# Optimization experiments

Measured on AMD Instinct MI355X. Metric: run time of the kernel, lower is better.

Reference implementation:

```python
import jax, jax.numpy as jnp
import numpy as np

N = 50000
E = 800000
IN_C = 128
HID = 16
HEADS = 8
OUT_C = 128
NEG_SLOPE = 0.2
EPS = 1e-16


def setup_inputs() -> dict:
    key = jax.random.key(0)
    ks = jax.random.split(key, 12)
    x = jax.random.normal(ks[0], (N, IN_C), dtype=jnp.float32)
    edge_index = jax.random.randint(ks[1], (2, E), 0, N, dtype=jnp.int32)
    s1 = 1.0 / np.sqrt(IN_C)
    s2 = 1.0 / np.sqrt(HID * HEADS)
    W1 = jax.random.normal(ks[2], (IN_C, HEADS * HID), dtype=jnp.float32) * s1
    att_src1 = jax.random.normal(ks[3], (HEADS, HID), dtype=jnp.float32) * s1
    att_dst1 = jax.random.normal(ks[4], (HEADS, HID), dtype=jnp.float32) * s1
    b1 = jnp.zeros((HEADS * HID,), dtype=jnp.float32)
    W2 = jax.random.normal(ks[5], (HEADS * HID, OUT_C), dtype=jnp.float32) * s2
    att_src2 = jax.random.normal(ks[6], (1, OUT_C), dtype=jnp.float32) * s2
    att_dst2 = jax.random.normal(ks[7], (1, OUT_C), dtype=jnp.float32) * s2
    b2 = jnp.zeros((OUT_C,), dtype=jnp.float32)
    return {"x": x, "edge_index": edge_index, "W1": W1, "att_src1": att_src1,
            "att_dst1": att_dst1, "b1": b1, "W2": W2, "att_src2": att_src2,
            "att_dst2": att_dst2, "b2": b2}


def _add_self_loops(edge_index, n):
    loop = jnp.arange(n, dtype=edge_index.dtype)
    src = jnp.concatenate([edge_index[0], loop])
    dst = jnp.concatenate([edge_index[1], loop])
    return src, dst


def gat_conv(x, src, dst, W, att_src, att_dst, bias, heads, out_c, concat):
    n = x.shape[0]
    h = (x @ W).reshape(n, heads, out_c)          # [N, H, C]
    a_src = jnp.einsum('nhc,hc->nh', h, att_src)  # [N, H]
    a_dst = jnp.einsum('nhc,hc->nh', h, att_dst)
    e = a_src[src] + a_dst[dst]                   # [E', H]
    e = jax.nn.leaky_relu(e, NEG_SLOPE)
    # segment softmax over edges grouped by destination node
    m = jax.ops.segment_max(e, dst, num_segments=n)          # [N, H]
    m = jnp.where(jnp.isfinite(m), m, 0.0)
    ex = jnp.exp(e - m[dst])                                  # [E', H]
    denom = jax.ops.segment_sum(ex, dst, num_segments=n)      # [N, H]
    alpha = ex / (denom[dst] + EPS)                            # [E', H]
    msg = alpha[:, :, None] * h[src]                           # [E', H, C]
    out = jax.ops.segment_sum(msg, dst, num_segments=n)       # [N, H, C]
    if concat:
        out = out.reshape(n, heads * out_c)
    else:
        out = out.mean(axis=1)
    return out + bias


def reference(x, edge_index, W1, att_src1, att_dst1, b1, W2, att_src2, att_dst2, b2):
    src, dst = _add_self_loops(edge_index, N)
    h = gat_conv(x, src, dst, W1, att_src1, att_dst1, b1, HEADS, HID, True)
    h = jax.nn.relu(h)
    # dropout is identity in eval mode
    out = gat_conv(h, src, dst, W2, att_src2, att_dst2, b2, 1, OUT_C, False)
    return out
```

## Files before the change

### kernel.cpp

```cpp
#include <hip/hip_runtime.h>


constexpr int N_NODES = 50000;
constexpr int E_EDGES = 800000;
constexpr int ETOT = E_EDGES + N_NODES;
constexpr float NEG_SLOPE = 0.2f;
constexpr float EPS = 1e-16f;
constexpr int SCAN_BLK = 512;
constexpr int NBLK_SCAN = (N_NODES + SCAN_BLK - 1) / SCAN_BLK;

typedef short bf16x8 __attribute__((ext_vector_type(8)));
typedef float f32x4 __attribute__((ext_vector_type(4)));

__device__ __forceinline__ float lrelu(float x) { return x > 0.f ? x : NEG_SLOPE * x; }
__device__ __forceinline__ ushort f2bf(float f) {
    uint u = __float_as_uint(f);
    return (ushort)((u + 0x7fffu + ((u >> 16) & 1u)) >> 16);
}
__device__ __forceinline__ float bf2f(uint u) { return __uint_as_float(u << 16); }

__device__ __forceinline__ void fma8(float* acc, uint4 p, float w, float& ws) {
    ws += w;
    acc[0] += w * bf2f(p.x & 0xffffu); acc[1] += w * bf2f(p.x >> 16);
    acc[2] += w * bf2f(p.y & 0xffffu); acc[3] += w * bf2f(p.y >> 16);
    acc[4] += w * bf2f(p.z & 0xffffu); acc[5] += w * bf2f(p.z >> 16);
    acc[6] += w * bf2f(p.w & 0xffffu); acc[7] += w * bf2f(p.w >> 16);
}

__global__ __launch_bounds__(256) void convert_W(const float* __restrict__ W1,
                                                 const float* __restrict__ W2,
                                                 const float* __restrict__ attS2,
                                                 const float* __restrict__ attD2,
                                                 ushort* __restrict__ W1t,
                                                 ushort* __restrict__ W2t,
                                                 float* __restrict__ vs,
                                                 float* __restrict__ vd,
                                                 uint* __restrict__ cnt16) {
    const int t = threadIdx.x;
    if (blockIdx.x >= 2) {
        const int i = (blockIdx.x - 2) * 256 + t;
        if (i < (N_NODES + 1) / 2) cnt16[i] = 0;
        return;
    }
    const float* W = (blockIdx.x == 0) ? W1 : W2;
    ushort* Wt = (blockIdx.x == 0) ? W1t : W2t;
    const int n = t >> 1, k0 = (t & 1) * 64;
    for (int k = 0; k < 64; k += 2) {
        uint lo = f2bf(W[(size_t)(k0 + k) * 128 + n]);
        uint hi = f2bf(W[(size_t)(k0 + k + 1) * 128 + n]);
        *(uint*)&Wt[(size_t)n * 128 + k0 + k] = lo | (hi << 16);
    }
    if (blockIdx.x == 1) {
        const int k = t & 127;
        const float* av = (t < 128) ? attS2 : attD2;
        float* dst = (t < 128) ? vs : vd;
        float s = 0.f;
        for (int c = 0; c < 128; ++c) s += W2[(size_t)k * 128 + c] * av[c];
        dst[k] = s;
    }
}

__device__ __forceinline__ uint cnt_at(const uint* cnt16, int i) {
    return (cnt16[i >> 1] >> ((i & 1) * 16)) & 0xffffu;
}

__global__ __launch_bounds__(SCAN_BLK) void block_sums(const uint* __restrict__ cnt16,
                                                       int* __restrict__ bsum) {
    __shared__ int sm[SCAN_BLK];
    int i = blockIdx.x * SCAN_BLK + threadIdx.x;
    sm[threadIdx.x] = (i < N_NODES) ? (int)cnt_at(cnt16, i) : 0;
    __syncthreads();
    for (int off = SCAN_BLK / 2; off > 0; off >>= 1) {
        if (threadIdx.x < off) sm[threadIdx.x] += sm[threadIdx.x + off];
        __syncthreads();
    }
    if (threadIdx.x == 0) bsum[blockIdx.x] = sm[0];
}

__global__ __launch_bounds__(SCAN_BLK) void scan_final_fused(const uint* __restrict__ cnt16,
                                                             const int* __restrict__ bsum,
                                                             int* __restrict__ rowptr) {
    __shared__ int sb[128];
    __shared__ int sm[SCAN_BLK];
    const int t = threadIdx.x;
    if (t < 128) sb[t] = (t < NBLK_SCAN) ? bsum[t] : 0;
    __syncthreads();
    for (int off = 1; off < 128; off <<= 1) {
        int v = 0;
        if (t < 128 && t >= off) v = sb[t - off];
        __syncthreads();
        if (t < 128) sb[t] += v;
        __syncthreads();
    }
    const int bid = blockIdx.x;
    const int bpre = sb[bid] - bsum[bid];

    const int i = bid * SCAN_BLK + t;
    const int v = (i < N_NODES) ? (int)cnt_at(cnt16, i) : 0;
    sm[t] = v;
    __syncthreads();
    for (int off = 1; off < SCAN_BLK; off <<= 1) {
        int x = (t >= off) ? sm[t - off] : 0;
        __syncthreads();
        sm[t] += x;
        __syncthreads();
    }
    if (i < N_NODES) rowptr[i] = bpre + sm[t] - v;
    if (bid == 0 && t == 0) rowptr[N_NODES] = ETOT;
}

__global__ __launch_bounds__(256) void scatter_kernel(const int* __restrict__ ei,
                                                      const int* __restrict__ rowptr,
                                                      const ushort* __restrict__ rank,
                                                      int* __restrict__ csrc) {
    int e = blockIdx.x * blockDim.x + threadIdx.x;
    if (e >= ETOT) return;
    int s, d;
    if (e < E_EDGES) { s = ei[e]; d = ei[E_EDGES + e]; }
    else             { s = d = e - E_EDGES; }
    const int pos = rowptr[d] + (int)rank[e];
    __builtin_nontemporal_store(s, &csrc[pos]);
}

template <bool BF16IN, bool ATT8, bool ATTIN>
__global__ __launch_bounds__(256) void mfma_gemm(const void* __restrict__ Xv,
                                                 const ushort* __restrict__ Wt,
                                                 ushort* __restrict__ H,
                                                 const float* __restrict__ attS,
                                                 const float* __restrict__ attD,
                                                 float* __restrict__ aS,
                                                 float* __restrict__ aD,
                                                 const int* __restrict__ ei,
                                                 uint* __restrict__ cnt16,
                                                 ushort* __restrict__ rank,
                                                 int cblocks, int nrows) {
    __shared__ __align__(16) char smem[16384 + 32768];
    ushort* lx = (ushort*)smem;
    ushort* lw = (ushort*)(smem + 16384);
    float*  hs = (float*)smem;

    const int t = threadIdx.x;

    if (blockIdx.x < cblocks) {
        const int e = blockIdx.x * 256 + t;
        if (e < ETOT) {
            const int d = (e < E_EDGES) ? ei[E_EDGES + e] : (e - E_EDGES);
            const uint shift = (d & 1) * 16;
            const uint old = atomicAdd(&cnt16[d >> 1], 1u << shift);
            rank[e] = (ushort)((old >> shift) & 0xffffu);
        }
        return;
    }

    const int r0 = (blockIdx.x - cblocks) * 64;

    {
        const int n = t >> 1, half = t & 1;
        const ushort* src = Wt + (size_t)n * 128 + half * 64;
        #pragma unroll
        for (int c = 0; c < 8; ++c) {
            int cx = half * 8 + c;
            uint4 v = *(const uint4*)(src + c * 8);
            *(uint4*)&lw[(n * 16 + (cx ^ (n & 7))) * 8] = v;
        }
    }
    {
        const int r = t >> 2, q = t & 3;
        const int grow = r0 + r;
        const uint4 z = {0, 0, 0, 0};
        #pragma unroll
        for (int cc = 0; cc < 4; ++cc) {
            int cx = q * 4 + cc;
            uint4 packed = z;
            if (grow < nrows) {
                if (BF16IN) {
                    packed = *(const uint4*)((const ushort*)Xv + (size_t)grow * 128 + cx * 8);
                } else {
                    const float* X = (const float*)Xv;
                    const float4 f0 = *(const float4*)(X + (size_t)grow * 128 + cx * 8);
                    const float4 f1 = *(const float4*)(X + (size_t)grow * 128 + cx * 8 + 4);
                    packed.x = (uint)f2bf(f0.x) | ((uint)f2bf(f0.y) << 16);
                    packed.y = (uint)f2bf(f0.z) | ((uint)f2bf(f0.w) << 16);
                    packed.z = (uint)f2bf(f1.x) | ((uint)f2bf(f1.y) << 16);
                    packed.w = (uint)f2bf(f1.z) | ((uint)f2bf(f1.w) << 16);
                }
            }
            *(uint4*)&lx[(r * 16 + (cx ^ (r & 7))) * 8] = packed;
        }
    }
    __syncthreads();

    const int wv = t >> 6, l = t & 63;
    const int row = wv * 16 + (l & 15);
    const int lg = l >> 4;
    f32x4 acc[8] = {};

    #pragma unroll
    for (int kb = 0; kb < 4; ++kb) {
        const int cx = kb * 4 + lg;
        bf16x8 a = *(const bf16x8*)&lx[(row * 16 + (cx ^ (row & 7))) * 8];
        #pragma unroll
        for (int nt = 0; nt < 8; ++nt) {
            const int n = nt * 16 + (l & 15);
            bf16x8 b = *(const bf16x8*)&lw[(n * 16 + (cx ^ (n & 7))) * 8];
            acc[nt] = __builtin_amdgcn_mfma_f32_16x16x32_bf16(a, b, acc[nt], 0, 0, 0);
        }
    }

    #pragma unroll
    for (int reg = 0; reg < 4; ++reg) {
        const int grow = r0 + wv * 16 + lg * 4 + reg;
        if (grow < nrows) {
            #pragma unroll
            for (int nt = 0; nt < 8; ++nt)
                H[(size_t)grow * 128 + nt * 16 + (l & 15)] = f2bf(acc[nt][reg]);
        }
    }

    if (ATT8) {
        __syncthreads();
        #pragma unroll
        for (int reg = 0; reg < 4; ++reg) {
            const int r = wv * 16 + lg * 4 + reg;
            #pragma unroll
            for (int nt = 0; nt < 8; ++nt)
                hs[r * 130 + nt * 16 + (l & 15)] = acc[nt][reg];
        }
        __syncthreads();
        for (int q = t; q < 512; q += 256) {
            const int r = q >> 3, h = q & 7;
            if (r0 + r < nrows) {
                float sv = 0.f, dv = 0.f;
                #pragma unroll
                for (int j = 0; j < 16; ++j) {
                    const float hv = hs[r * 130 + h * 16 + j];
                    sv += hv * attS[h * 16 + j];
                    dv += hv * attD[h * 16 + j];
                }
                aS[(size_t)(r0 + r) * 8 + h] = sv;
                aD[(size_t)(r0 + r) * 8 + h] = dv;
            }
        }
    }

    if (ATTIN) {
        const int r = t >> 2, qq = t & 3;
        float ps = 0.f, pd = 0.f;
        #pragma unroll
        for (int cc = 0; cc < 4; ++cc) {
            const int cx = qq * 4 + cc;
            const uint4 p = *(const uint4*)&lx[(r * 16 + (cx ^ (r & 7))) * 8];
            const uint w[4] = {p.x, p.y, p.z, p.w};
            #pragma unroll
            for (int q = 0; q < 4; ++q) {
                const float e0 = bf2f(w[q] & 0xffffu);
                const float e1 = bf2f(w[q] >> 16);
                ps += e0 * attS[cx * 8 + 2 * q] + e1 * attS[cx * 8 + 2 * q + 1];
                pd += e0 * attD[cx * 8 + 2 * q] + e1 * attD[cx * 8 + 2 * q + 1];
            }
        }
        ps += __shfl_xor(ps, 1); ps += __shfl_xor(ps, 2);
        pd += __shfl_xor(pd, 1); pd += __shfl_xor(pd, 2);
        if (qq == 0 && r0 + r < nrows) { aS[r0 + r] = ps; aD[r0 + r] = pd; }
    }
}

#define GISSUE(P, JJ)                                                          \
    {                                                                          \
        const int jx_ = (JJ);                                                  \
        const int sx_ = __shfl(s_l, jx_ & 63);                                 \
        P = zero4;                                                             \
        if (jx_ < rem) P = *(const uint4*)(Hm + (size_t)sx_ * 128 + i * 8);    \
    }

__global__ __launch_bounds__(256) void agg8(const int* __restrict__ rowptr,
                                            const int* __restrict__ csrc,
                                            const float* __restrict__ aS,
                                            const float* __restrict__ aD,
                                            const ushort* __restrict__ Hm,
                                            const float* __restrict__ bias,
                                            ushort* __restrict__ o1bf) {
    __shared__ float wlds[4][512];
    const int wv = threadIdx.x >> 6;
    const int d = blockIdx.x * 4 + wv;
    const int lane = threadIdx.x & 63;
    const int g = lane >> 4, i = lane & 15, hc = i >> 1;
    const int hw = lane & 7;
    const float adh = aD[(size_t)d * 8 + hw];

    const int base = rowptr[d], end = rowptr[d + 1];
    float acc[8] = {0.f, 0.f, 0.f, 0.f, 0.f, 0.f, 0.f, 0.f};
    float ws = 0.f;
    const uint4 zero4 = {0, 0, 0, 0};

    for (int c0 = base; c0 < end; c0 += 64) {
        const int rem = min(64, end - c0);
        const int s_l = (lane < rem) ? csrc[c0 + lane] : 0;

        uint4 p0, p1, p2, p3;
        GISSUE(p0, g); GISSUE(p1, g + 4); GISSUE(p2, g + 8); GISSUE(p3, g + 12);

        const int nwc = (rem + 7) >> 3;
        for (int jj = 0; jj < nwc; ++jj) {
            const int j = jj * 8 + (lane >> 3);
            const int sj = __shfl(s_l, j & 63);
            float w = 0.f;
            if (j < rem) w = __expf(lrelu(aS[(size_t)sj * 8 + hw] + adh));
            wlds[wv][j * 8 + hw] = w;
        }

        const int niter = (rem + 3) >> 2;
        for (int tb = 0; tb < niter; tb += 4) {
            const int j0 = 4 * tb + g;
            {
                const float w = (j0 < rem) ? wlds[wv][j0 * 8 + hc] : 0.f;
                fma8(acc, p0, w, ws);
                GISSUE(p0, j0 + 16);
            }
            {
                const int j1 = j0 + 4;
                const float w = (j1 < rem) ? wlds[wv][j1 * 8 + hc] : 0.f;
                fma8(acc, p1, w, ws);
                GISSUE(p1, j1 + 16);
            }
            {
                const int j2 = j0 + 8;
                const float w = (j2 < rem) ? wlds[wv][j2 * 8 + hc] : 0.f;
                fma8(acc, p2, w, ws);
                GISSUE(p2, j2 + 16);
            }
            {
                const int j3 = j0 + 12;
                const float w = (j3 < rem) ? wlds[wv][j3 * 8 + hc] : 0.f;
                fma8(acc, p3, w, ws);
                GISSUE(p3, j3 + 16);
            }
        }
    }

    #pragma unroll
    for (int k = 0; k < 8; ++k) {
        acc[k] += __shfl_xor(acc[k], 16);
        acc[k] += __shfl_xor(acc[k], 32);
    }
    ws += __shfl_xor(ws, 16);
    ws += __shfl_xor(ws, 32);

    if (g == 0) {
        const float inv = 1.f / (ws + EPS);
        float v[8];
        #pragma unroll
        for (int k = 0; k < 8; ++k) v[k] = fmaxf(acc[k] * inv + bias[i * 8 + k], 0.f);
        uint4 pk;
        pk.x = (uint)f2bf(v[0]) | ((uint)f2bf(v[1]) << 16);
        pk.y = (uint)f2bf(v[2]) | ((uint)f2bf(v[3]) << 16);
        pk.z = (uint)f2bf(v[4]) | ((uint)f2bf(v[5]) << 16);
        pk.w = (uint)f2bf(v[6]) | ((uint)f2bf(v[7]) << 16);
        *(uint4*)(o1bf + (size_t)d * 128 + i * 8) = pk;
    }
}

__global__ __launch_bounds__(256) void agg1(const int* __restrict__ rowptr,
                                            const int* __restrict__ csrc,
                                            const float* __restrict__ aS,
                                            const float* __restrict__ aD,
                                            const ushort* __restrict__ Hm,
                                            const float* __restrict__ bias,
                                            float* __restrict__ out) {
    const int wv = threadIdx.x >> 6;
    const int d = blockIdx.x * 4 + wv;
    const int lane = threadIdx.x & 63;
    const int g = lane >> 4, i = lane & 15;
    const float ad = aD[d];

    const int base = rowptr[d], end = rowptr[d + 1];
    float acc[8] = {0.f, 0.f, 0.f, 0.f, 0.f, 0.f, 0.f, 0.f};
    float ws = 0.f;
    const uint4 zero4 = {0, 0, 0, 0};

    for (int c0 = base; c0 < end; c0 += 64) {
        const int rem = min(64, end - c0);
        const int s_l = (lane < rem) ? csrc[c0 + lane] : 0;

        uint4 p0, p1, p2, p3;
        GISSUE(p0, g); GISSUE(p1, g + 4); GISSUE(p2, g + 8); GISSUE(p3, g + 12);

        const float w_l = (lane < rem) ? __expf(lrelu(aS[s_l] + ad)) : 0.f;

        const int niter = (rem + 3) >> 2;
        for (int tb = 0; tb < niter; tb += 4) {
            const int j0 = 4 * tb + g;
            {
                const float wr = __shfl(w_l, j0 & 63);
                const float w = (j0 < rem) ? wr : 0.f;
                fma8(acc, p0, w, ws);
                GISSUE(p0, j0 + 16);
            }
            {
                const int j1 = j0 + 4;
                const float wr = __shfl(w_l, j1 & 63);
                const float w = (j1 < rem) ? wr : 0.f;
                fma8(acc, p1, w, ws);
                GISSUE(p1, j1 + 16);
            }
            {
                const int j2 = j0 + 8;
                const float wr = __shfl(w_l, j2 & 63);
                const float w = (j2 < rem) ? wr : 0.f;
                fma8(acc, p2, w, ws);
                GISSUE(p2, j2 + 16);
            }
            {
                const int j3 = j0 + 12;
                const float wr = __shfl(w_l, j3 & 63);
                const float w = (j3 < rem) ? wr : 0.f;
                fma8(acc, p3, w, ws);
                GISSUE(p3, j3 + 16);
            }
        }
    }

    #pragma unroll
    for (int k = 0; k < 8; ++k) {
        acc[k] += __shfl_xor(acc[k], 16);
        acc[k] += __shfl_xor(acc[k], 32);
    }
    ws += __shfl_xor(ws, 16);
    ws += __shfl_xor(ws, 32);

    if (g == 0) {
        const float inv = 1.f / (ws + EPS);
        float4 o0, o1v;
        o0.x = acc[0] * inv + bias[i * 8 + 0];
        o0.y = acc[1] * inv + bias[i * 8 + 1];
        o0.z = acc[2] * inv + bias[i * 8 + 2];
        o0.w = acc[3] * inv + bias[i * 8 + 3];
        o1v.x = acc[4] * inv + bias[i * 8 + 4];
        o1v.y = acc[5] * inv + bias[i * 8 + 5];
        o1v.z = acc[6] * inv + bias[i * 8 + 6];
        o1v.w = acc[7] * inv + bias[i * 8 + 7];
        *(float4*)(out + (size_t)d * 128 + i * 8) = o0;
        *(float4*)(out + (size_t)d * 128 + i * 8 + 4) = o1v;
    }
}

extern "C" void kernel_launch(void* const* d_in, const int* in_sizes, int n_in,
                              void* d_out, int out_size, void* d_ws, size_t ws_size,
                              hipStream_t stream) {
    const float* x        = (const float*)d_in[0];
    const int*   ei       = (const int*)  d_in[1];
    const float* W1       = (const float*)d_in[2];
    const float* att_src1 = (const float*)d_in[3];
    const float* att_dst1 = (const float*)d_in[4];
    const float* b1       = (const float*)d_in[5];
    const float* W2       = (const float*)d_in[6];
    const float* att_src2 = (const float*)d_in[7];
    const float* att_dst2 = (const float*)d_in[8];
    const float* b2       = (const float*)d_in[9];
    float* out = (float*)d_out;

    ushort* Hbf  = (ushort*)d_ws;
    ushort* o1bf = Hbf + (size_t)N_NODES * 128;
    float*  aS1  = (float*)(o1bf + (size_t)N_NODES * 128);
    float*  aD1  = aS1 + (size_t)N_NODES * 8;
    float*  aS2  = aD1 + (size_t)N_NODES * 8;
    float*  aD2  = aS2 + N_NODES;
    float*  vs   = aD2 + N_NODES;
    float*  vd   = vs + 128;
    ushort* W1t  = (ushort*)(vd + 128);
    ushort* W2t  = W1t + 128 * 128;
    uint* cnt16  = (uint*)(W2t + 128 * 128);
    int* rowptr  = (int*)(cnt16 + (N_NODES + 1) / 2 + 1);
    int* bsum    = rowptr + N_NODES + 1;
    ushort* rank = (ushort*)(bsum + 128);
    int* csrc    = (int*)(rank + ETOT + 2);

    const int zblk = ((N_NODES + 1) / 2 + 255) / 256;
    const int eblk = (ETOT + 255) / 256;
    const int gemm_blocks = (N_NODES + 63) / 64;
    const int agg_blocks = N_NODES / 4;

    convert_W<<<2 + zblk, 256, 0, stream>>>(W1, W2, att_src2, att_dst2,
                                            W1t, W2t, vs, vd, cnt16);

    mfma_gemm<false, true, false><<<eblk + gemm_blocks, 256, 0, stream>>>(
        x, W1t, Hbf, att_src1, att_dst1, aS1, aD1, ei, cnt16, rank, eblk, N_NODES);

    block_sums<<<NBLK_SCAN, SCAN_BLK, 0, stream>>>(cnt16, bsum);
    scan_final_fused<<<NBLK_SCAN, SCAN_BLK, 0, stream>>>(cnt16, bsum, rowptr);
    scatter_kernel<<<eblk, 256, 0, stream>>>(ei, rowptr, rank, csrc);

    agg8<<<agg_blocks, 256, 0, stream>>>(rowptr, csrc, aS1, aD1, Hbf, b1, o1bf);

    mfma_gemm<true, false, true><<<gemm_blocks, 256, 0, stream>>>(
        o1bf, W2t, Hbf, vs, vd, aS2, aD2, nullptr, nullptr, nullptr, 0, N_NODES);

    agg1<<<agg_blocks, 256, 0, stream>>>(rowptr, csrc, aS2, aD2, Hbf, b2, out);
}
```

Measured before the change: 216.6 us.

## Compress CSR source indices to 16-bit, pack FMAs, split count kernel out of GEMM

Stores CSR source indices as ushort instead of int, halving index traffic in scatter and both aggregation kernels. Because N_NODES is 50000, every index fits in 16 bits, but the encoding only holds for graphs below 65536 nodes. Accumulation is rewritten as packed float2 FMAs via elementwise_fma. The degree-count and rank atomics move out of the fused first GEMM into a separate count_rank kernel, and the first GEMM now runs after the CSR build. agg1 now reads edge weights from LDS instead of wave shuffles.

```diff
diff --git a/kernel.cpp b/kernel.cpp
--- a/kernel.cpp
+++ b/kernel.cpp
@@ -11,6 +11,7 @@
 
 typedef short bf16x8 __attribute__((ext_vector_type(8)));
 typedef float f32x4 __attribute__((ext_vector_type(4)));
+typedef float f32x2 __attribute__((ext_vector_type(2)));
 
 __device__ __forceinline__ float lrelu(float x) { return x > 0.f ? x : NEG_SLOPE * x; }
 __device__ __forceinline__ ushort f2bf(float f) {
@@ -19,12 +20,20 @@
 }
 __device__ __forceinline__ float bf2f(uint u) { return __uint_as_float(u << 16); }
 
-__device__ __forceinline__ void fma8(float* acc, uint4 p, float w, float& ws) {
+__device__ __forceinline__ void fma_pair(f32x2& acc, uint u, f32x2 w2) {
+    f32x2 h;
+    h.x = __uint_as_float(u << 16);
+    h.y = __uint_as_float(u & 0xffff0000u);
+    acc = __builtin_elementwise_fma(h, w2, acc);
+}
+
+__device__ __forceinline__ void fma8v(f32x2* acc, uint4 p, float w, float& ws) {
     ws += w;
-    acc[0] += w * bf2f(p.x & 0xffffu); acc[1] += w * bf2f(p.x >> 16);
-    acc[2] += w * bf2f(p.y & 0xffffu); acc[3] += w * bf2f(p.y >> 16);
-    acc[4] += w * bf2f(p.z & 0xffffu); acc[5] += w * bf2f(p.z >> 16);
-    acc[6] += w * bf2f(p.w & 0xffffu); acc[7] += w * bf2f(p.w >> 16);
+    const f32x2 w2 = {w, w};
+    fma_pair(acc[0], p.x, w2);
+    fma_pair(acc[1], p.y, w2);
+    fma_pair(acc[2], p.z, w2);
+    fma_pair(acc[3], p.w, w2);
 }
 
 __global__ __launch_bounds__(256) void convert_W(const float* __restrict__ W1,
@@ -60,6 +69,17 @@
     }
 }
 
+__global__ __launch_bounds__(256) void count_rank(const int* __restrict__ ei,
+                                                  uint* __restrict__ cnt16,
+                                                  ushort* __restrict__ rank) {
+    int e = blockIdx.x * blockDim.x + threadIdx.x;
+    if (e >= ETOT) return;
+    int d = (e < E_EDGES) ? ei[E_EDGES + e] : (e - E_EDGES);
+    const uint shift = (d & 1) * 16;
+    uint old = atomicAdd(&cnt16[d >> 1], 1u << shift);
+    rank[e] = (ushort)((old >> shift) & 0xffffu);
+}
+
 __device__ __forceinline__ uint cnt_at(const uint* cnt16, int i) {
     return (cnt16[i >> 1] >> ((i & 1) * 16)) & 0xffffu;
 }
@@ -112,14 +132,14 @@
 __global__ __launch_bounds__(256) void scatter_kernel(const int* __restrict__ ei,
                                                       const int* __restrict__ rowptr,
                                                       const ushort* __restrict__ rank,
-                                                      int* __restrict__ csrc) {
+                                                      ushort* __restrict__ csrc) {
     int e = blockIdx.x * blockDim.x + threadIdx.x;
     if (e >= ETOT) return;
     int s, d;
     if (e < E_EDGES) { s = ei[e]; d = ei[E_EDGES + e]; }
     else             { s = d = e - E_EDGES; }
     const int pos = rowptr[d] + (int)rank[e];
-    __builtin_nontemporal_store(s, &csrc[pos]);
+    __builtin_nontemporal_store((ushort)s, &csrc[pos]);
 }
 
 template <bool BF16IN, bool ATT8, bool ATTIN>
@@ -130,29 +150,14 @@
                                                  const float* __restrict__ attD,
                                                  float* __restrict__ aS,
                                                  float* __restrict__ aD,
-                                                 const int* __restrict__ ei,
-                                                 uint* __restrict__ cnt16,
-                                                 ushort* __restrict__ rank,
-                                                 int cblocks, int nrows) {
+                                                 int nrows) {
     __shared__ __align__(16) char smem[16384 + 32768];
     ushort* lx = (ushort*)smem;
     ushort* lw = (ushort*)(smem + 16384);
     float*  hs = (float*)smem;
 
     const int t = threadIdx.x;
-
-    if (blockIdx.x < cblocks) {
-        const int e = blockIdx.x * 256 + t;
-        if (e < ETOT) {
-            const int d = (e < E_EDGES) ? ei[E_EDGES + e] : (e - E_EDGES);
-            const uint shift = (d & 1) * 16;
-            const uint old = atomicAdd(&cnt16[d >> 1], 1u << shift);
-            rank[e] = (ushort)((old >> shift) & 0xffffu);
-        }
-        return;
-    }
-
-    const int r0 = (blockIdx.x - cblocks) * 64;
+    const int r0 = blockIdx.x * 64;
 
     {
         const int n = t >> 1, half = t & 1;
@@ -274,7 +279,7 @@
     }
 
 __global__ __launch_bounds__(256) void agg8(const int* __restrict__ rowptr,
-                                            const int* __restrict__ csrc,
+                                            const ushort* __restrict__ csrc,
                                             const float* __restrict__ aS,
                                             const float* __restrict__ aD,
                                             const ushort* __restrict__ Hm,
@@ -289,13 +294,13 @@
     const float adh = aD[(size_t)d * 8 + hw];
 
     const int base = rowptr[d], end = rowptr[d + 1];
-    float acc[8] = {0.f, 0.f, 0.f, 0.f, 0.f, 0.f, 0.f, 0.f};
+    f32x2 acc[4] = {{0.f, 0.f}, {0.f, 0.f}, {0.f, 0.f}, {0.f, 0.f}};
     float ws = 0.f;
     const uint4 zero4 = {0, 0, 0, 0};
 
     for (int c0 = base; c0 < end; c0 += 64) {
         const int rem = min(64, end - c0);
-        const int s_l = (lane < rem) ? csrc[c0 + lane] : 0;
+        const int s_l = (lane < rem) ? (int)csrc[c0 + lane] : 0;
 
         uint4 p0, p1, p2, p3;
         GISSUE(p0, g); GISSUE(p1, g + 4); GISSUE(p2, g + 8); GISSUE(p3, g + 12);
@@ -314,34 +319,34 @@
             const int j0 = 4 * tb + g;
             {
                 const float w = (j0 < rem) ? wlds[wv][j0 * 8 + hc] : 0.f;
-                fma8(acc, p0, w, ws);
+                fma8v(acc, p0, w, ws);
                 GISSUE(p0, j0 + 16);
             }
             {
                 const int j1 = j0 + 4;
                 const float w = (j1 < rem) ? wlds[wv][j1 * 8 + hc] : 0.f;
-                fma8(acc, p1, w, ws);
+                fma8v(acc, p1, w, ws);
                 GISSUE(p1, j1 + 16);
             }
             {
                 const int j2 = j0 + 8;
                 const float w = (j2 < rem) ? wlds[wv][j2 * 8 + hc] : 0.f;
-                fma8(acc, p2, w, ws);
+                fma8v(acc, p2, w, ws);
                 GISSUE(p2, j2 + 16);
             }
             {
                 const int j3 = j0 + 12;
                 const float w = (j3 < rem) ? wlds[wv][j3 * 8 + hc] : 0.f;
-                fma8(acc, p3, w, ws);
+                fma8v(acc, p3, w, ws);
                 GISSUE(p3, j3 + 16);
             }
         }
     }
 
     #pragma unroll
-    for (int k = 0; k < 8; ++k) {
-        acc[k] += __shfl_xor(acc[k], 16);
-        acc[k] += __shfl_xor(acc[k], 32);
+    for (int k = 0; k < 4; ++k) {
+        acc[k].x += __shfl_xor(acc[k].x, 16); acc[k].x += __shfl_xor(acc[k].x, 32);
+        acc[k].y += __shfl_xor(acc[k].y, 16); acc[k].y += __shfl_xor(acc[k].y, 32);
     }
     ws += __shfl_xor(ws, 16);
     ws += __shfl_xor(ws, 32);
@@ -350,7 +355,10 @@
         const float inv = 1.f / (ws + EPS);
         float v[8];
         #pragma unroll
-        for (int k = 0; k < 8; ++k) v[k] = fmaxf(acc[k] * inv + bias[i * 8 + k], 0.f);
+        for (int k = 0; k < 4; ++k) {
+            v[2 * k]     = fmaxf(acc[k].x * inv + bias[i * 8 + 2 * k], 0.f);
+            v[2 * k + 1] = fmaxf(acc[k].y * inv + bias[i * 8 + 2 * k + 1], 0.f);
+        }
         uint4 pk;
         pk.x = (uint)f2bf(v[0]) | ((uint)f2bf(v[1]) << 16);
         pk.y = (uint)f2bf(v[2]) | ((uint)f2bf(v[3]) << 16);
@@ -361,12 +369,13 @@
 }
 
 __global__ __launch_bounds__(256) void agg1(const int* __restrict__ rowptr,
-                                            const int* __restrict__ csrc,
+                                            const ushort* __restrict__ csrc,
                                             const float* __restrict__ aS,
                                             const float* __restrict__ aD,
                                             const ushort* __restrict__ Hm,
                                             const float* __restrict__ bias,
                                             float* __restrict__ out) {
+    __shared__ float wlds[4][64];
     const int wv = threadIdx.x >> 6;
     const int d = blockIdx.x * 4 + wv;
     const int lane = threadIdx.x & 63;
@@ -374,56 +383,52 @@
     const float ad = aD[d];
 
     const int base = rowptr[d], end = rowptr[d + 1];
-    float acc[8] = {0.f, 0.f, 0.f, 0.f, 0.f, 0.f, 0.f, 0.f};
+    f32x2 acc[4] = {{0.f, 0.f}, {0.f, 0.f}, {0.f, 0.f}, {0.f, 0.f}};
     float ws = 0.f;
     const uint4 zero4 = {0, 0, 0, 0};
 
     for (int c0 = base; c0 < end; c0 += 64) {
         const int rem = min(64, end - c0);
-        const int s_l = (lane < rem) ? csrc[c0 + lane] : 0;
+        const int s_l = (lane < rem) ? (int)csrc[c0 + lane] : 0;
 
         uint4 p0, p1, p2, p3;
         GISSUE(p0, g); GISSUE(p1, g + 4); GISSUE(p2, g + 8); GISSUE(p3, g + 12);
 
-        const float w_l = (lane < rem) ? __expf(lrelu(aS[s_l] + ad)) : 0.f;
+        wlds[wv][lane] = (lane < rem) ? __expf(lrelu(aS[s_l] + ad)) : 0.f;
 
         const int niter = (rem + 3) >> 2;
         for (int tb = 0; tb < niter; tb += 4) {
             const int j0 = 4 * tb + g;
             {
-                const float wr = __shfl(w_l, j0 & 63);
-                const float w = (j0 < rem) ? wr : 0.f;
-                fma8(acc, p0, w, ws);
+                const float w = (j0 < rem) ? wlds[wv][j0] : 0.f;
+                fma8v(acc, p0, w, ws);
                 GISSUE(p0, j0 + 16);
             }
             {
                 const int j1 = j0 + 4;
-                const float wr = __shfl(w_l, j1 & 63);
-                const float w = (j1 < rem) ? wr : 0.f;
-                fma8(acc, p1, w, ws);
+                const float w = (j1 < rem) ? wlds[wv][j1] : 0.f;
+                fma8v(acc, p1, w, ws);
                 GISSUE(p1, j1 + 16);
             }
             {
                 const int j2 = j0 + 8;
-                const float wr = __shfl(w_l, j2 & 63);
-                const float w = (j2 < rem) ? wr : 0.f;
-                fma8(acc, p2, w, ws);
+                const float w = (j2 < rem) ? wlds[wv][j2] : 0.f;
+                fma8v(acc, p2, w, ws);
                 GISSUE(p2, j2 + 16);
             }
             {
                 const int j3 = j0 + 12;
-                const float wr = __shfl(w_l, j3 & 63);
-                const float w = (j3 < rem) ? wr : 0.f;
-                fma8(acc, p3, w, ws);
+                const float w = (j3 < rem) ? wlds[wv][j3] : 0.f;
+                fma8v(acc, p3, w, ws);
                 GISSUE(p3, j3 + 16);
             }
         }
     }
 
     #pragma unroll
-    for (int k = 0; k < 8; ++k) {
-        acc[k] += __shfl_xor(acc[k], 16);
-        acc[k] += __shfl_xor(acc[k], 32);
+    for (int k = 0; k < 4; ++k) {
+        acc[k].x += __shfl_xor(acc[k].x, 16); acc[k].x += __shfl_xor(acc[k].x, 32);
+        acc[k].y += __shfl_xor(acc[k].y, 16); acc[k].y += __shfl_xor(acc[k].y, 32);
     }
     ws += __shfl_xor(ws, 16);
     ws += __shfl_xor(ws, 32);
@@ -431,14 +436,14 @@
     if (g == 0) {
         const float inv = 1.f / (ws + EPS);
         float4 o0, o1v;
-        o0.x = acc[0] * inv + bias[i * 8 + 0];
-        o0.y = acc[1] * inv + bias[i * 8 + 1];
-        o0.z = acc[2] * inv + bias[i * 8 + 2];
-        o0.w = acc[3] * inv + bias[i * 8 + 3];
-        o1v.x = acc[4] * inv + bias[i * 8 + 4];
-        o1v.y = acc[5] * inv + bias[i * 8 + 5];
-        o1v.z = acc[6] * inv + bias[i * 8 + 6];
-        o1v.w = acc[7] * inv + bias[i * 8 + 7];
+        o0.x = acc[0].x * inv + bias[i * 8 + 0];
+        o0.y = acc[0].y * inv + bias[i * 8 + 1];
+        o0.z = acc[1].x * inv + bias[i * 8 + 2];
+        o0.w = acc[1].y * inv + bias[i * 8 + 3];
+        o1v.x = acc[2].x * inv + bias[i * 8 + 4];
+        o1v.y = acc[2].y * inv + bias[i * 8 + 5];
+        o1v.z = acc[3].x * inv + bias[i * 8 + 6];
+        o1v.w = acc[3].y * inv + bias[i * 8 + 7];
         *(float4*)(out + (size_t)d * 128 + i * 8) = o0;
         *(float4*)(out + (size_t)d * 128 + i * 8 + 4) = o1v;
     }
@@ -473,7 +478,7 @@
     int* rowptr  = (int*)(cnt16 + (N_NODES + 1) / 2 + 1);
     int* bsum    = rowptr + N_NODES + 1;
     ushort* rank = (ushort*)(bsum + 128);
-    int* csrc    = (int*)(rank + ETOT + 2);
+    ushort* csrc = rank + ETOT + 2;
 
     const int zblk = ((N_NODES + 1) / 2 + 255) / 256;
     const int eblk = (ETOT + 255) / 256;
@@ -482,18 +487,16 @@
 
     convert_W<<<2 + zblk, 256, 0, stream>>>(W1, W2, att_src2, att_dst2,
                                             W1t, W2t, vs, vd, cnt16);
-
-    mfma_gemm<false, true, false><<<eblk + gemm_blocks, 256, 0, stream>>>(
-        x, W1t, Hbf, att_src1, att_dst1, aS1, aD1, ei, cnt16, rank, eblk, N_NODES);
-
+    count_rank<<<eblk, 256, 0, stream>>>(ei, cnt16, rank);
     block_sums<<<NBLK_SCAN, SCAN_BLK, 0, stream>>>(cnt16, bsum);
     scan_final_fused<<<NBLK_SCAN, SCAN_BLK, 0, stream>>>(cnt16, bsum, rowptr);
     scatter_kernel<<<eblk, 256, 0, stream>>>(ei, rowptr, rank, csrc);
 
+    mfma_gemm<false, true, false><<<gemm_blocks, 256, 0, stream>>>(
+        x, W1t, Hbf, att_src1, att_dst1, aS1, aD1, N_NODES);
     agg8<<<agg_blocks, 256, 0, stream>>>(rowptr, csrc, aS1, aD1, Hbf, b1, o1bf);
 
     mfma_gemm<true, false, true><<<gemm_blocks, 256, 0, stream>>>(
-        o1bf, W2t, Hbf, vs, vd, aS2, aD2, nullptr, nullptr, nullptr, 0, N_NODES);
-
+        o1bf, W2t, Hbf, vs, vd, aS2, aD2, N_NODES);
     agg1<<<agg_blocks, 256, 0, stream>>>(rowptr, csrc, aS2, aD2, Hbf, b2, out);
 }
```

Measured after the change: 217.4 us. Within noise of the previous version (+0.4%).
